# Kernel optimization log

Hardware: AMD Instinct MI355X
Metric: run time of the kernel (lower is better)

The kernel has to match this reference:

```python
import jax, jax.numpy as jnp
import numpy as np

B, S, V, E, H, T = 128, 512, 6000, 100, 256, 9


def setup_inputs() -> dict:
    key = jax.random.key(0)
    ks = jax.random.split(key, 16)
    lengths = jax.random.randint(ks[0], (B,), S // 4, S + 1)
    mask = (jnp.arange(S)[None, :] < lengths[:, None])  # [B,S] bool, contiguous prefixes
    data = jax.random.randint(ks[1], (B, S), 1, V)
    data = jnp.where(mask, data, 0)  # pad token = 0 (padding_idx)
    sc = 0.1
    emb = jax.random.normal(ks[2], (V, E), jnp.float32) * sc
    emb = emb.at[0].set(0.0)  # padding_idx=0
    return {
        "data": data, "mask": mask,
        "emb": emb,
        "W_ih_f": jax.random.normal(ks[3], (4 * H, E), jnp.float32) * sc,
        "W_hh_f": jax.random.normal(ks[4], (4 * H, H), jnp.float32) * sc,
        "b_f": jax.random.normal(ks[5], (4 * H,), jnp.float32) * sc,
        "W_ih_b": jax.random.normal(ks[6], (4 * H, E), jnp.float32) * sc,
        "W_hh_b": jax.random.normal(ks[7], (4 * H, H), jnp.float32) * sc,
        "b_b": jax.random.normal(ks[8], (4 * H,), jnp.float32) * sc,
        "mlp_W": jax.random.normal(ks[9], (T, 2 * H), jnp.float32) * sc,
        "mlp_b": jax.random.normal(ks[10], (T,), jnp.float32) * sc,
        "start_trans": jax.random.normal(ks[11], (T,), jnp.float32) * sc,
        "trans": jax.random.normal(ks[12], (T, T), jnp.float32) * sc,
        "end_trans": jax.random.normal(ks[13], (T,), jnp.float32) * sc,
    }


def _lstm_dir(xg, W_hh, reverse):
    # xg: [S,B,4H] precomputed input projection + biases
    h0 = jnp.zeros((xg.shape[1], W_hh.shape[1]), xg.dtype)

    def step(carry, xt):
        h, c = carry
        g = xt + h @ W_hh.T
        i, f, gg, o = jnp.split(g, 4, axis=-1)  # PyTorch gate order i,f,g,o
        c = jax.nn.sigmoid(f) * c + jax.nn.sigmoid(i) * jnp.tanh(gg)
        h = jax.nn.sigmoid(o) * jnp.tanh(c)
        return (h, c), h

    _, hs = jax.lax.scan(step, (h0, h0), xg, reverse=reverse)
    return hs  # [S,B,H]


def _emissions(data, emb, W_ih_f, W_hh_f, b_f, W_ih_b, W_hh_b, b_b, mlp_W, mlp_b):
    x = emb[data]  # [B,S,E]
    xg_f = jnp.einsum('bse,ge->sbg', x, W_ih_f) + b_f
    xg_b = jnp.einsum('bse,ge->sbg', x, W_ih_b) + b_b
    hf = _lstm_dir(xg_f, W_hh_f, False)
    hb = _lstm_dir(xg_b, W_hh_b, True)
    h = jnp.concatenate([hf, hb], axis=-1)  # [S,B,2H]
    return jnp.einsum('sbh,th->bst', h, mlp_W) + mlp_b  # [B,S,T]


def _viterbi(em, mask, start_trans, trans, end_trans):
    b, s, t = em.shape
    score0 = start_trans + em[:, 0]  # [B,T]
    em_t = jnp.swapaxes(em, 0, 1)[1:]      # [S-1,B,T]
    mask_t = jnp.swapaxes(mask, 0, 1)[1:]  # [S-1,B]

    def step(score, inp):
        e_t, m_t = inp
        cand = score[:, :, None] + trans[None] + e_t[:, None, :]  # [B,Tprev,Tcur]
        new = cand.max(axis=1)
        bp = cand.argmax(axis=1).astype(jnp.int32)  # [B,T]
        score = jnp.where(m_t[:, None], new, score)
        return score, bp

    score, bps = jax.lax.scan(step, score0, (em_t, mask_t))
    final = score + end_trans
    best_score = final.max(axis=-1)               # [B]
    last_tag = final.argmax(axis=-1).astype(jnp.int32)

    def back(tag, inp):
        bp, m_t = inp
        prev = jnp.take_along_axis(bp, tag[:, None], axis=1)[:, 0]
        prev = jnp.where(m_t, prev, tag)
        return prev, tag

    first_tag, tags_rest = jax.lax.scan(back, last_tag, (bps, mask_t), reverse=True)
    paths = jnp.concatenate([first_tag[None], tags_rest], axis=0)  # [S,B]
    paths = jnp.where(jnp.swapaxes(mask, 0, 1), paths, 0)
    return jnp.swapaxes(paths, 0, 1), best_score


def reference(data, mask, emb, W_ih_f, W_hh_f, b_f, W_ih_b, W_hh_b, b_b,
              mlp_W, mlp_b, start_trans, trans, end_trans):
    em = _emissions(data, emb, W_ih_f, W_hh_f, b_f, W_ih_b, W_hh_b, b_b, mlp_W, mlp_b)
    paths, best_score = _viterbi(em, mask, start_trans, trans, end_trans)
    return paths, best_score
```

## Files before the change

### kernel.cpp

```cpp
#include <hip/hip_runtime.h>
#include <math.h>
#include <stdint.h>

#define B 128
#define S 512
#define V 6000
#define E 100
#define H 256
#define G4 1024
#define T 9

#define WREG 18
#define WLDS 3
#define WSTR 43

#define OFF_PEMB_F 0u
#define PEMB_BYTES (V*G4*4u)
#define OFF_PEMB_B (OFF_PEMB_F + PEMB_BYTES)
#define OFF_EMF    (OFF_PEMB_B + PEMB_BYTES)
#define EM_BYTES   (B*S*T*4u)
#define OFF_EMB    (OFF_EMF + EM_BYTES)
#define OFF_BP     (OFF_EMB + EM_BYTES)
#define BP_BYTES   ((S-1)*B*16u)
#define OFF_LT     (OFF_BP + BP_BYTES)
#define OFF_PT     (OFF_LT + 512u)
#define OFF_WSTREAM OFF_BP

__device__ __forceinline__ float sigf(float x) { return 1.0f / (1.0f + expf(-x)); }

__global__ __launch_bounds__(256) void k_pemb(const float* __restrict__ emb,
                                              const float* __restrict__ wf, const float* __restrict__ bf,
                                              const float* __restrict__ wb, const float* __restrict__ bb,
                                              char* __restrict__ ws) {
    int blk = blockIdx.x;
    int d   = blk >= 375;
    int vb  = d ? blk - 375 : blk;
    const float* W    = d ? wb : wf;
    const float* bias = d ? bb : bf;
    float* pe = (float*)(ws + (d ? OFF_PEMB_B : OFF_PEMB_F));

    __shared__ float es[16 * E];
    for (int i = threadIdx.x; i < 16 * E; i += 256) es[i] = emb[vb * 16 * E + i];
    __syncthreads();

    int j = threadIdx.x;
    float acc[4][16];
    #pragma unroll
    for (int q = 0; q < 4; q++) {
        float bq = bias[q * H + j];
        #pragma unroll
        for (int v = 0; v < 16; v++) acc[q][v] = bq;
    }
    for (int e = 0; e < E; e++) {
        float w0 = W[(0 * H + j) * E + e];
        float w1 = W[(1 * H + j) * E + e];
        float w2 = W[(2 * H + j) * E + e];
        float w3 = W[(3 * H + j) * E + e];
        #pragma unroll
        for (int v = 0; v < 16; v++) {
            float x = es[v * E + e];
            acc[0][v] += w0 * x; acc[1][v] += w1 * x;
            acc[2][v] += w2 * x; acc[3][v] += w3 * x;
        }
    }
    for (int v = 0; v < 16; v++)
        #pragma unroll
        for (int q = 0; q < 4; q++)
            pe[(vb * 16 + v) * G4 + q * H + j] = acc[q][v];
}

__global__ __launch_bounds__(256) void k_prep(const float* __restrict__ whhf,
                                              const float* __restrict__ whhb,
                                              char* __restrict__ ws) {
    int tid = blockIdx.x * 256 + threadIdx.x;
    if (tid >= 2 * WSTR * 1024) return;
    int d   = tid >= WSTR * 1024;
    int idx = d ? tid - WSTR * 1024 : tid;
    int g = idx >> 10, r = idx & 1023;
    const float* whh = d ? whhb : whhf;
    float4* wstr = (float4*)(ws + OFF_WSTREAM);
    const float4* src = (const float4*)(whh + (size_t)r * H + 4 * (WREG + WLDS));
    wstr[((size_t)(d * WSTR + g) << 10) + r] = src[g];
}

__global__ __launch_bounds__(512, 2) void k_lstm(const int* __restrict__ data,
                                                 const float* __restrict__ whhf,
                                                 const float* __restrict__ whhb,
                                                 const float* __restrict__ mlpW,
                                                 char* __restrict__ ws) {
    int blk = blockIdx.x;
    int d = blk >> 7, b = blk & 127;
    const float* whh = d ? whhb : whhf;
    const float* pe  = (const float*)(ws + (d ? OFF_PEMB_B : OFF_PEMB_F));
    float* emdst = (float*)(ws + (d ? OFF_EMB : OFF_EMF));
    const float4* wstr = (const float4*)(ws + OFF_WSTREAM) + ((size_t)(d * WSTR) << 10);

    __shared__ __align__(16) float hs[H];
    __shared__ float4 sW[WLDS << 10];
    __shared__ float  gbuf[G4];
    __shared__ float  red[T][4];
    __shared__ int    toks[S];

    int t = threadIdx.x;
    int r0 = t, r1 = t + 512;

    const float4* wrow0 = (const float4*)(whh + (size_t)r0 * H);
    const float4* wrow1 = (const float4*)(whh + (size_t)r1 * H);
    float4 wA[WREG], wB[WREG];
    #pragma unroll
    for (int g = 0; g < WREG; g++) { wA[g] = wrow0[g]; wB[g] = wrow1[g]; }
    #pragma unroll
    for (int g = 0; g < WLDS; g++) {
        sW[(g << 10) + r0] = wrow0[WREG + g];
        sW[(g << 10) + r1] = wrow1[WREG + g];
    }

    toks[t] = data[b * S + t];

    float mw[T];
    if (t < 256) {
        #pragma unroll
        for (int tt = 0; tt < T; tt++) mw[tt] = mlpW[tt * (2 * H) + d * H + t];
    }
    if (t < H) hs[t] = 0.0f;
    float cst = 0.0f;
    __syncthreads();

    const float4* hs4 = (const float4*)hs;
    const float4* wsp0 = wstr + r0;
    const float4* wsp1 = wstr + r1;

    float pf0, pf1;
    {
        int sp0 = d ? (S - 1) : 0;
        size_t tok = (size_t)toks[sp0];
        pf0 = pe[(tok << 10) + r0];
        pf1 = pe[(tok << 10) + r1];
    }

    for (int ss = 0; ss < S; ss++) {
        int sp = d ? (S - 1 - ss) : ss;
        float acc0 = pf0, acc1 = pf1;
        if (ss + 1 < S) {
            int spn = d ? (S - 2 - ss) : (ss + 1);
            size_t tok = (size_t)toks[spn];
            pf0 = pe[(tok << 10) + r0];
            pf1 = pe[(tok << 10) + r1];
        }

        #pragma unroll
        for (int g = 0; g < WREG; g++) {
            float4 h4 = hs4[g];
            float4 a = wA[g], bb2 = wB[g];
            acc0 = fmaf(a.x, h4.x, acc0);  acc1 = fmaf(bb2.x, h4.x, acc1);
            acc0 = fmaf(a.y, h4.y, acc0);  acc1 = fmaf(bb2.y, h4.y, acc1);
            acc0 = fmaf(a.z, h4.z, acc0);  acc1 = fmaf(bb2.z, h4.z, acc1);
            acc0 = fmaf(a.w, h4.w, acc0);  acc1 = fmaf(bb2.w, h4.w, acc1);
        }
        #pragma unroll
        for (int g = 0; g < WLDS; g++) {
            float4 w0 = sW[(g << 10) + r0];
            float4 w1 = sW[(g << 10) + r1];
            float4 h4 = hs4[WREG + g];
            acc0 = fmaf(w0.x, h4.x, acc0);  acc1 = fmaf(w1.x, h4.x, acc1);
            acc0 = fmaf(w0.y, h4.y, acc0);  acc1 = fmaf(w1.y, h4.y, acc1);
            acc0 = fmaf(w0.z, h4.z, acc0);  acc1 = fmaf(w1.z, h4.z, acc1);
            acc0 = fmaf(w0.w, h4.w, acc0);  acc1 = fmaf(w1.w, h4.w, acc1);
        }
        #pragma unroll 4
        for (int g = 0; g < WSTR; g++) {
            float4 w0 = wsp0[(size_t)g << 10];
            float4 w1 = wsp1[(size_t)g << 10];
            float4 h4 = hs4[WREG + WLDS + g];
            acc0 = fmaf(w0.x, h4.x, acc0);  acc1 = fmaf(w1.x, h4.x, acc1);
            acc0 = fmaf(w0.y, h4.y, acc0);  acc1 = fmaf(w1.y, h4.y, acc1);
            acc0 = fmaf(w0.z, h4.z, acc0);  acc1 = fmaf(w1.z, h4.z, acc1);
            acc0 = fmaf(w0.w, h4.w, acc0);  acc1 = fmaf(w1.w, h4.w, acc1);
        }
        gbuf[r0] = acc0;
        gbuf[r1] = acc1;
        __syncthreads();

        if (t < 256) {
            float gi = gbuf[t], gf = gbuf[H + t], gg = gbuf[2 * H + t], go = gbuf[3 * H + t];
            float ig = sigf(gi), fg = sigf(gf), tg = tanhf(gg), og = sigf(go);
            cst = fg * cst + ig * tg;
            float hn = og * tanhf(cst);
            hs[t] = hn;
            int l = t & 63, wv = t >> 6;
            #pragma unroll
            for (int tt = 0; tt < T; tt++) {
                float v = hn * mw[tt];
                v += __shfl_xor(v, 32, 64); v += __shfl_xor(v, 16, 64);
                v += __shfl_xor(v, 8, 64);  v += __shfl_xor(v, 4, 64);
                v += __shfl_xor(v, 2, 64);  v += __shfl_xor(v, 1, 64);
                if (l == 0) red[tt][wv] = v;
            }
        }
        __syncthreads();
        if (t < T)
            emdst[((size_t)b * S + sp) * T + t] = red[t][0] + red[t][1] + red[t][2] + red[t][3];
    }
}

__global__ __launch_bounds__(64) void k_vit(const int* __restrict__ data,
                                            const float* __restrict__ strans,
                                            const float* __restrict__ trans,
                                            const float* __restrict__ etrans,
                                            const float* __restrict__ mlpb,
                                            float* __restrict__ out,
                                            char* __restrict__ ws) {
    int b = blockIdx.x, t = threadIdx.x;
    const float* emf = (const float*)(ws + OFF_EMF);
    const float* emb = (const float*)(ws + OFF_EMB);
    char* bp = ws + OFF_BP;
    int*  lt = (int*)(ws + OFF_LT);
    bool act = t < T;

    float trp[T];
    float mb = 0.0f;
    if (act) {
        #pragma unroll
        for (int p = 0; p < T; p++) trp[p] = trans[p * T + t];
        mb = mlpb[t];
    }
    float score = -1e30f;
    if (act) score = strans[t] + emf[(b * S) * T + t] + emb[(b * S) * T + t] + mb;

    for (int s = 1; s < S; s++) {
        float e = 0.0f;
        if (act) e = emf[(b * S + s) * T + t] + emb[(b * S + s) * T + t] + mb;
        float best = __shfl(score, 0, 64) + trp[0];
        int bpi = 0;
        #pragma unroll
        for (int p = 1; p < T; p++) {
            float cand = __shfl(score, p, 64) + trp[p];
            if (cand > best) { best = cand; bpi = p; }
        }
        int m = data[b * S + s] != 0;
        if (act) {
            score = m ? (best + e) : score;
            bp[((size_t)(s - 1) * B + b) * 16 + t] = (char)bpi;
        }
    }
    float fin = act ? score + etrans[t] : -1e30f;
    float bv = __shfl(fin, 0, 64);
    int bi = 0;
    #pragma unroll
    for (int p = 1; p < T; p++) {
        float v = __shfl(fin, p, 64);
        if (v > bv) { bv = v; bi = p; }
    }
    if (t == 0) { out[B * S + b] = bv; lt[b] = bi; }
}

__global__ __launch_bounds__(128) void k_back(const int* __restrict__ data, char* __restrict__ ws) {
    int b = threadIdx.x;
    const int4* bp4 = (const int4*)(ws + OFF_BP);
    const int*  lt  = (const int*)(ws + OFF_LT);
    int* pt = (int*)(ws + OFF_PT);
    int tag = lt[b];
    pt[(S - 1) * B + b] = tag;
    for (int p = S - 2; p >= 0; p--) {
        int4 r = bp4[(size_t)p * B + b];
        int m = data[b * S + p + 1] != 0;
        unsigned w = (unsigned)(tag < 8 ? (tag < 4 ? r.x : r.y) : r.z);
        int nt = (int)((w >> ((tag & 3) * 8)) & 0xff);
        tag = m ? nt : tag;
        pt[p * B + b] = tag;
    }
}

__global__ __launch_bounds__(256) void k_fin(const int* __restrict__ data,
                                             float* __restrict__ out,
                                             const char* __restrict__ ws) {
    int tid = blockIdx.x * 256 + threadIdx.x;
    const int* pt = (const int*)(ws + OFF_PT);
    int b = tid >> 9, p = tid & 511;
    out[tid] = (data[tid] != 0) ? (float)pt[p * B + b] : 0.0f;
}

extern "C" void kernel_launch(void* const* d_in, const int* in_sizes, int n_in,
                              void* d_out, int out_size, void* d_ws, size_t ws_size,
                              hipStream_t stream) {
    const int*   data = (const int*)d_in[0];
    const float* emb  = (const float*)d_in[2];
    const float* wihf = (const float*)d_in[3];
    const float* whhf = (const float*)d_in[4];
    const float* bf   = (const float*)d_in[5];
    const float* wihb = (const float*)d_in[6];
    const float* whhb = (const float*)d_in[7];
    const float* bb   = (const float*)d_in[8];
    const float* mlpW = (const float*)d_in[9];
    const float* mlpb = (const float*)d_in[10];
    const float* st   = (const float*)d_in[11];
    const float* tr   = (const float*)d_in[12];
    const float* et   = (const float*)d_in[13];
    float* out = (float*)d_out;
    char*  ws  = (char*)d_ws;

    hipLaunchKernelGGL(k_pemb, dim3(750),  dim3(256), 0, stream, emb, wihf, bf, wihb, bb, ws);
    hipLaunchKernelGGL(k_prep, dim3(344),  dim3(256), 0, stream, whhf, whhb, ws);
    hipLaunchKernelGGL(k_lstm, dim3(256),  dim3(512), 0, stream, data, whhf, whhb, mlpW, ws);
    hipLaunchKernelGGL(k_vit,  dim3(128),  dim3(64),  0, stream, data, st, tr, et, mlpb, out, ws);
    hipLaunchKernelGGL(k_back, dim3(1),    dim3(128), 0, stream, data, ws);
    hipLaunchKernelGGL(k_fin,  dim3(256),  dim3(256), 0, stream, data, out, ws);
}
```

Measured before the change: 5.145 ms.

## Remap LSTM to one thread per hidden unit with AGPR-resident weights

The recurrent kernel now runs 256 threads per block, and each thread computes all four gates of one hidden unit. This removes the gate exchange buffer and one barrier's worth of cross-thread work. Recurrent weights sit in three tiers: a slice in VGPRs, a larger slice parked in accumulation registers (AGPRs) via inline asm, and a small slice in LDS. Only the remaining columns are streamed from the regrouped global copy, which cuts global and L2 weight traffic per step. The risks are fewer waves to hide latency, extra accvgpr read instructions, and register pressure from the inline asm.

```diff
diff --git a/kernel.cpp b/kernel.cpp
--- a/kernel.cpp
+++ b/kernel.cpp
@@ -10,9 +10,11 @@
 #define G4 1024
 #define T 9
 
-#define WREG 18
-#define WLDS 3
-#define WSTR 43
+#define NVG 9
+#define NAG 16
+#define NLD 3
+#define NST 36
+#define GST (NVG + NAG + NLD)
 
 #define OFF_PEMB_F 0u
 #define PEMB_BYTES (V*G4*4u)
@@ -73,17 +75,19 @@
                                               const float* __restrict__ whhb,
                                               char* __restrict__ ws) {
     int tid = blockIdx.x * 256 + threadIdx.x;
-    if (tid >= 2 * WSTR * 1024) return;
-    int d   = tid >= WSTR * 1024;
-    int idx = d ? tid - WSTR * 1024 : tid;
-    int g = idx >> 10, r = idx & 1023;
+    if (tid >= 2 * 4 * NST * 256) return;
+    int d   = tid >= 4 * NST * 256;
+    int idx = d ? tid - 4 * NST * 256 : tid;
+    int q  = idx / (NST * 256);
+    int r2 = idx % (NST * 256);
+    int gi = r2 >> 8, j = r2 & 255;
     const float* whh = d ? whhb : whhf;
     float4* wstr = (float4*)(ws + OFF_WSTREAM);
-    const float4* src = (const float4*)(whh + (size_t)r * H + 4 * (WREG + WLDS));
-    wstr[((size_t)(d * WSTR + g) << 10) + r] = src[g];
-}
-
-__global__ __launch_bounds__(512, 2) void k_lstm(const int* __restrict__ data,
+    const float4* src = (const float4*)(whh + (size_t)(q * H + j) * H);
+    wstr[((size_t)((d * 4 + q) * NST + gi) << 8) + j] = src[GST + gi];
+}
+
+__global__ __launch_bounds__(256, 1) void k_lstm(const int* __restrict__ data,
                                                  const float* __restrict__ whhf,
                                                  const float* __restrict__ whhb,
                                                  const float* __restrict__ mlpW,
@@ -93,109 +97,161 @@
     const float* whh = d ? whhb : whhf;
     const float* pe  = (const float*)(ws + (d ? OFF_PEMB_B : OFF_PEMB_F));
     float* emdst = (float*)(ws + (d ? OFF_EMB : OFF_EMF));
-    const float4* wstr = (const float4*)(ws + OFF_WSTREAM) + ((size_t)(d * WSTR) << 10);
+    const float4* wstr = (const float4*)(ws + OFF_WSTREAM);
 
     __shared__ __align__(16) float hs[H];
-    __shared__ float4 sW[WLDS << 10];
-    __shared__ float  gbuf[G4];
+    __shared__ float4 sW[NLD * 4 * 256];
     __shared__ float  red[T][4];
     __shared__ int    toks[S];
 
     int t = threadIdx.x;
-    int r0 = t, r1 = t + 512;
-
-    const float4* wrow0 = (const float4*)(whh + (size_t)r0 * H);
-    const float4* wrow1 = (const float4*)(whh + (size_t)r1 * H);
-    float4 wA[WREG], wB[WREG];
-    #pragma unroll
-    for (int g = 0; g < WREG; g++) { wA[g] = wrow0[g]; wB[g] = wrow1[g]; }
-    #pragma unroll
-    for (int g = 0; g < WLDS; g++) {
-        sW[(g << 10) + r0] = wrow0[WREG + g];
-        sW[(g << 10) + r1] = wrow1[WREG + g];
-    }
+
+    float4 wv[NVG * 4];
+    #pragma unroll
+    for (int g = 0; g < NVG; g++)
+        #pragma unroll
+        for (int q = 0; q < 4; q++)
+            wv[g * 4 + q] = ((const float4*)(whh + (size_t)(q * H + t) * H))[g];
+    #pragma unroll
+    for (int i = 0; i < NVG * 4; i++)
+        asm volatile("" : "+v"(wv[i].x), "+v"(wv[i].y), "+v"(wv[i].z), "+v"(wv[i].w));
+
+    float ag[NAG * 4 * 4];
+    #pragma unroll
+    for (int g = 0; g < NAG; g++)
+        #pragma unroll
+        for (int q = 0; q < 4; q++) {
+            float4 w = ((const float4*)(whh + (size_t)(q * H + t) * H))[NVG + g];
+            int base = (g * 4 + q) * 4;
+            asm volatile("v_accvgpr_write_b32 %0, %1" : "=a"(ag[base + 0]) : "v"(w.x));
+            asm volatile("v_accvgpr_write_b32 %0, %1" : "=a"(ag[base + 1]) : "v"(w.y));
+            asm volatile("v_accvgpr_write_b32 %0, %1" : "=a"(ag[base + 2]) : "v"(w.z));
+            asm volatile("v_accvgpr_write_b32 %0, %1" : "=a"(ag[base + 3]) : "v"(w.w));
+        }
+
+    #pragma unroll
+    for (int g = 0; g < NLD; g++)
+        #pragma unroll
+        for (int q = 0; q < 4; q++)
+            sW[((g * 4 + q) << 8) + t] = ((const float4*)(whh + (size_t)(q * H + t) * H))[NVG + NAG + g];
 
     toks[t] = data[b * S + t];
+    toks[t + 256] = data[b * S + t + 256];
 
     float mw[T];
-    if (t < 256) {
-        #pragma unroll
-        for (int tt = 0; tt < T; tt++) mw[tt] = mlpW[tt * (2 * H) + d * H + t];
-    }
-    if (t < H) hs[t] = 0.0f;
+    #pragma unroll
+    for (int tt = 0; tt < T; tt++) mw[tt] = mlpW[tt * (2 * H) + d * H + t];
+
+    hs[t] = 0.0f;
     float cst = 0.0f;
     __syncthreads();
 
     const float4* hs4 = (const float4*)hs;
-    const float4* wsp0 = wstr + r0;
-    const float4* wsp1 = wstr + r1;
-
-    float pf0, pf1;
+    const float4* ws0 = wstr + (((size_t)(d * 4 + 0) * NST) << 8) + t;
+    const float4* ws1 = wstr + (((size_t)(d * 4 + 1) * NST) << 8) + t;
+    const float4* ws2 = wstr + (((size_t)(d * 4 + 2) * NST) << 8) + t;
+    const float4* ws3 = wstr + (((size_t)(d * 4 + 3) * NST) << 8) + t;
+
+    float pf0, pf1, pf2, pf3;
     {
         int sp0 = d ? (S - 1) : 0;
         size_t tok = (size_t)toks[sp0];
-        pf0 = pe[(tok << 10) + r0];
-        pf1 = pe[(tok << 10) + r1];
+        pf0 = pe[(tok << 10) + 0 * H + t];
+        pf1 = pe[(tok << 10) + 1 * H + t];
+        pf2 = pe[(tok << 10) + 2 * H + t];
+        pf3 = pe[(tok << 10) + 3 * H + t];
     }
 
     for (int ss = 0; ss < S; ss++) {
         int sp = d ? (S - 1 - ss) : ss;
-        float acc0 = pf0, acc1 = pf1;
+        float a0 = pf0, a1 = pf1, a2 = pf2, a3 = pf3;
         if (ss + 1 < S) {
             int spn = d ? (S - 2 - ss) : (ss + 1);
             size_t tok = (size_t)toks[spn];
-            pf0 = pe[(tok << 10) + r0];
-            pf1 = pe[(tok << 10) + r1];
-        }
-
-        #pragma unroll
-        for (int g = 0; g < WREG; g++) {
+            pf0 = pe[(tok << 10) + 0 * H + t];
+            pf1 = pe[(tok << 10) + 1 * H + t];
+            pf2 = pe[(tok << 10) + 2 * H + t];
+            pf3 = pe[(tok << 10) + 3 * H + t];
+        }
+
+        #pragma unroll
+        for (int g = 0; g < NVG; g++) {
             float4 h4 = hs4[g];
-            float4 a = wA[g], bb2 = wB[g];
-            acc0 = fmaf(a.x, h4.x, acc0);  acc1 = fmaf(bb2.x, h4.x, acc1);
-            acc0 = fmaf(a.y, h4.y, acc0);  acc1 = fmaf(bb2.y, h4.y, acc1);
-            acc0 = fmaf(a.z, h4.z, acc0);  acc1 = fmaf(bb2.z, h4.z, acc1);
-            acc0 = fmaf(a.w, h4.w, acc0);  acc1 = fmaf(bb2.w, h4.w, acc1);
-        }
-        #pragma unroll
-        for (int g = 0; g < WLDS; g++) {
-            float4 w0 = sW[(g << 10) + r0];
-            float4 w1 = sW[(g << 10) + r1];
-            float4 h4 = hs4[WREG + g];
-            acc0 = fmaf(w0.x, h4.x, acc0);  acc1 = fmaf(w1.x, h4.x, acc1);
-            acc0 = fmaf(w0.y, h4.y, acc0);  acc1 = fmaf(w1.y, h4.y, acc1);
-            acc0 = fmaf(w0.z, h4.z, acc0);  acc1 = fmaf(w1.z, h4.z, acc1);
-            acc0 = fmaf(w0.w, h4.w, acc0);  acc1 = fmaf(w1.w, h4.w, acc1);
+            float4 w0 = wv[g * 4 + 0], w1 = wv[g * 4 + 1],
+                   w2 = wv[g * 4 + 2], w3 = wv[g * 4 + 3];
+            a0 = fmaf(w0.x, h4.x, a0); a0 = fmaf(w0.y, h4.y, a0);
+            a0 = fmaf(w0.z, h4.z, a0); a0 = fmaf(w0.w, h4.w, a0);
+            a1 = fmaf(w1.x, h4.x, a1); a1 = fmaf(w1.y, h4.y, a1);
+            a1 = fmaf(w1.z, h4.z, a1); a1 = fmaf(w1.w, h4.w, a1);
+            a2 = fmaf(w2.x, h4.x, a2); a2 = fmaf(w2.y, h4.y, a2);
+            a2 = fmaf(w2.z, h4.z, a2); a2 = fmaf(w2.w, h4.w, a2);
+            a3 = fmaf(w3.x, h4.x, a3); a3 = fmaf(w3.y, h4.y, a3);
+            a3 = fmaf(w3.z, h4.z, a3); a3 = fmaf(w3.w, h4.w, a3);
+        }
+        #pragma unroll
+        for (int g = 0; g < NAG; g++) {
+            float4 h4 = hs4[NVG + g];
+            #pragma unroll
+            for (int q = 0; q < 4; q++) {
+                int base = (g * 4 + q) * 4;
+                float w0, w1, w2, w3;
+                asm volatile("v_accvgpr_read_b32 %0, %1" : "=v"(w0) : "a"(ag[base + 0]));
+                asm volatile("v_accvgpr_read_b32 %0, %1" : "=v"(w1) : "a"(ag[base + 1]));
+                asm volatile("v_accvgpr_read_b32 %0, %1" : "=v"(w2) : "a"(ag[base + 2]));
+                asm volatile("v_accvgpr_read_b32 %0, %1" : "=v"(w3) : "a"(ag[base + 3]));
+                float acc = (q == 0) ? a0 : (q == 1) ? a1 : (q == 2) ? a2 : a3;
+                acc = fmaf(w0, h4.x, acc); acc = fmaf(w1, h4.y, acc);
+                acc = fmaf(w2, h4.z, acc); acc = fmaf(w3, h4.w, acc);
+                if (q == 0) a0 = acc; else if (q == 1) a1 = acc;
+                else if (q == 2) a2 = acc; else a3 = acc;
+            }
+        }
+        #pragma unroll
+        for (int g = 0; g < NLD; g++) {
+            float4 h4 = hs4[NVG + NAG + g];
+            float4 w0 = sW[((g * 4 + 0) << 8) + t], w1 = sW[((g * 4 + 1) << 8) + t];
+            float4 w2 = sW[((g * 4 + 2) << 8) + t], w3 = sW[((g * 4 + 3) << 8) + t];
+            a0 = fmaf(w0.x, h4.x, a0); a0 = fmaf(w0.y, h4.y, a0);
+            a0 = fmaf(w0.z, h4.z, a0); a0 = fmaf(w0.w, h4.w, a0);
+            a1 = fmaf(w1.x, h4.x, a1); a1 = fmaf(w1.y, h4.y, a1);
+            a1 = fmaf(w1.z, h4.z, a1); a1 = fmaf(w1.w, h4.w, a1);
+            a2 = fmaf(w2.x, h4.x, a2); a2 = fmaf(w2.y, h4.y, a2);
+            a2 = fmaf(w2.z, h4.z, a2); a2 = fmaf(w2.w, h4.w, a2);
+            a3 = fmaf(w3.x, h4.x, a3); a3 = fmaf(w3.y, h4.y, a3);
+            a3 = fmaf(w3.z, h4.z, a3); a3 = fmaf(w3.w, h4.w, a3);
         }
         #pragma unroll 4
-        for (int g = 0; g < WSTR; g++) {
-            float4 w0 = wsp0[(size_t)g << 10];
-            float4 w1 = wsp1[(size_t)g << 10];
-            float4 h4 = hs4[WREG + WLDS + g];
-            acc0 = fmaf(w0.x, h4.x, acc0);  acc1 = fmaf(w1.x, h4.x, acc1);
-            acc0 = fmaf(w0.y, h4.y, acc0);  acc1 = fmaf(w1.y, h4.y, acc1);
-            acc0 = fmaf(w0.z, h4.z, acc0);  acc1 = fmaf(w1.z, h4.z, acc1);
-            acc0 = fmaf(w0.w, h4.w, acc0);  acc1 = fmaf(w1.w, h4.w, acc1);
-        }
-        gbuf[r0] = acc0;
-        gbuf[r1] = acc1;
+        for (int gs = 0; gs < NST; gs++) {
+            float4 w0 = ws0[gs << 8];
+            float4 w1 = ws1[gs << 8];
+            float4 w2 = ws2[gs << 8];
+            float4 w3 = ws3[gs << 8];
+            float4 h4 = hs4[GST + gs];
+            a0 = fmaf(w0.x, h4.x, a0); a0 = fmaf(w0.y, h4.y, a0);
+            a0 = fmaf(w0.z, h4.z, a0); a0 = fmaf(w0.w, h4.w, a0);
+            a1 = fmaf(w1.x, h4.x, a1); a1 = fmaf(w1.y, h4.y, a1);
+            a1 = fmaf(w1.z, h4.z, a1); a1 = fmaf(w1.w, h4.w, a1);
+            a2 = fmaf(w2.x, h4.x, a2); a2 = fmaf(w2.y, h4.y, a2);
+            a2 = fmaf(w2.z, h4.z, a2); a2 = fmaf(w2.w, h4.w, a2);
+            a3 = fmaf(w3.x, h4.x, a3); a3 = fmaf(w3.y, h4.y, a3);
+            a3 = fmaf(w3.z, h4.z, a3); a3 = fmaf(w3.w, h4.w, a3);
+        }
+
+        float ig = sigf(a0), fg = sigf(a1), tg = tanhf(a2), og = sigf(a3);
+        cst = fg * cst + ig * tg;
+        float hn = og * tanhf(cst);
+
         __syncthreads();
-
-        if (t < 256) {
-            float gi = gbuf[t], gf = gbuf[H + t], gg = gbuf[2 * H + t], go = gbuf[3 * H + t];
-            float ig = sigf(gi), fg = sigf(gf), tg = tanhf(gg), og = sigf(go);
-            cst = fg * cst + ig * tg;
-            float hn = og * tanhf(cst);
-            hs[t] = hn;
-            int l = t & 63, wv = t >> 6;
-            #pragma unroll
-            for (int tt = 0; tt < T; tt++) {
-                float v = hn * mw[tt];
-                v += __shfl_xor(v, 32, 64); v += __shfl_xor(v, 16, 64);
-                v += __shfl_xor(v, 8, 64);  v += __shfl_xor(v, 4, 64);
-                v += __shfl_xor(v, 2, 64);  v += __shfl_xor(v, 1, 64);
-                if (l == 0) red[tt][wv] = v;
-            }
+        hs[t] = hn;
+
+        int l = t & 63, wv2 = t >> 6;
+        #pragma unroll
+        for (int tt = 0; tt < T; tt++) {
+            float v = hn * mw[tt];
+            v += __shfl_xor(v, 32, 64); v += __shfl_xor(v, 16, 64);
+            v += __shfl_xor(v, 8, 64);  v += __shfl_xor(v, 4, 64);
+            v += __shfl_xor(v, 2, 64);  v += __shfl_xor(v, 1, 64);
+            if (l == 0) red[tt][wv2] = v;
         }
         __syncthreads();
         if (t < T)
@@ -300,8 +356,8 @@
     char*  ws  = (char*)d_ws;
 
     hipLaunchKernelGGL(k_pemb, dim3(750),  dim3(256), 0, stream, emb, wihf, bf, wihb, bb, ws);
-    hipLaunchKernelGGL(k_prep, dim3(344),  dim3(256), 0, stream, whhf, whhb, ws);
-    hipLaunchKernelGGL(k_lstm, dim3(256),  dim3(512), 0, stream, data, whhf, whhb, mlpW, ws);
+    hipLaunchKernelGGL(k_prep, dim3(288),  dim3(256), 0, stream, whhf, whhb, ws);
+    hipLaunchKernelGGL(k_lstm, dim3(256),  dim3(256), 0, stream, data, whhf, whhb, mlpW, ws);
     hipLaunchKernelGGL(k_vit,  dim3(128),  dim3(64),  0, stream, data, st, tr, et, mlpb, out, ws);
     hipLaunchKernelGGL(k_back, dim3(1),    dim3(128), 0, stream, data, ws);
     hipLaunchKernelGGL(k_fin,  dim3(256),  dim3(256), 0, stream, data, out, ws);
```

New measurement: 7.457 ms. 45.0% more time.

## Hold recurrent weights in AGPRs and enlarge LDS weight cache to cut streaming

Applied to the files above, without the earlier changes.

Rebalances where the recurrent W_hh rows live in the LSTM kernel. 16 float4 groups per row now sit in accumulator registers (written and read through inline asm), 9 groups sit in about 147 KB of dynamic LDS, and only 39 groups are streamed from global memory each step instead of 43. The prep kernel and its grid are resized to match. The aim is less per-step global/L2 traffic on the serial recurrence. In exchange it adds AGPR read instructions, and the large LDS footprint limits the kernel to one block per CU. It also sets the dynamic-LDS attribute on every host call.

```diff
diff --git a/kernel.cpp b/kernel.cpp
--- a/kernel.cpp
+++ b/kernel.cpp
@@ -10,9 +10,17 @@
 #define G4 1024
 #define T 9
 
-#define WREG 18
-#define WLDS 3
-#define WSTR 43
+#define NAGR 16
+#define NLDR 9
+#define NSTR 39
+#define GSTR (NAGR + NLDR)
+
+#define SM_W    0u
+#define SM_HS   147456u
+#define SM_GB   148480u
+#define SM_RED  152576u
+#define SM_TOK  152720u
+#define SM_SIZE 154768u
 
 #define OFF_PEMB_F 0u
 #define PEMB_BYTES (V*G4*4u)
@@ -73,14 +81,14 @@
                                               const float* __restrict__ whhb,
                                               char* __restrict__ ws) {
     int tid = blockIdx.x * 256 + threadIdx.x;
-    if (tid >= 2 * WSTR * 1024) return;
-    int d   = tid >= WSTR * 1024;
-    int idx = d ? tid - WSTR * 1024 : tid;
-    int g = idx >> 10, r = idx & 1023;
+    if (tid >= 2 * NSTR * 1024) return;
+    int d   = tid >= NSTR * 1024;
+    int idx = d ? tid - NSTR * 1024 : tid;
+    int gi = idx >> 10, r = idx & 1023;
     const float* whh = d ? whhb : whhf;
     float4* wstr = (float4*)(ws + OFF_WSTREAM);
-    const float4* src = (const float4*)(whh + (size_t)r * H + 4 * (WREG + WLDS));
-    wstr[((size_t)(d * WSTR + g) << 10) + r] = src[g];
+    const float4* src = (const float4*)(whh + (size_t)r * H);
+    wstr[((size_t)(d * NSTR + gi) << 10) + r] = src[GSTR + gi];
 }
 
 __global__ __launch_bounds__(512, 2) void k_lstm(const int* __restrict__ data,
@@ -88,31 +96,43 @@
                                                  const float* __restrict__ whhb,
                                                  const float* __restrict__ mlpW,
                                                  char* __restrict__ ws) {
+    extern __shared__ char smem[];
+    float4* sW  = (float4*)(smem + SM_W);
+    float*  hs  = (float*)(smem + SM_HS);
+    float*  gbuf= (float*)(smem + SM_GB);
+    float (*red)[4] = (float(*)[4])(smem + SM_RED);
+    int*    toks= (int*)(smem + SM_TOK);
+
     int blk = blockIdx.x;
     int d = blk >> 7, b = blk & 127;
     const float* whh = d ? whhb : whhf;
     const float* pe  = (const float*)(ws + (d ? OFF_PEMB_B : OFF_PEMB_F));
     float* emdst = (float*)(ws + (d ? OFF_EMB : OFF_EMF));
-    const float4* wstr = (const float4*)(ws + OFF_WSTREAM) + ((size_t)(d * WSTR) << 10);
-
-    __shared__ __align__(16) float hs[H];
-    __shared__ float4 sW[WLDS << 10];
-    __shared__ float  gbuf[G4];
-    __shared__ float  red[T][4];
-    __shared__ int    toks[S];
+    const float4* wstrD = (const float4*)(ws + OFF_WSTREAM) + ((size_t)(d * NSTR) << 10);
 
     int t = threadIdx.x;
     int r0 = t, r1 = t + 512;
-
     const float4* wrow0 = (const float4*)(whh + (size_t)r0 * H);
     const float4* wrow1 = (const float4*)(whh + (size_t)r1 * H);
-    float4 wA[WREG], wB[WREG];
+
+    float agA[NAGR * 4], agB[NAGR * 4];
     #pragma unroll
-    for (int g = 0; g < WREG; g++) { wA[g] = wrow0[g]; wB[g] = wrow1[g]; }
+    for (int g = 0; g < NAGR; g++) {
+        float4 wa = wrow0[g];
+        float4 wb2 = wrow1[g];
+        asm volatile("v_accvgpr_write_b32 %0, %1" : "=a"(agA[g * 4 + 0]) : "v"(wa.x));
+        asm volatile("v_accvgpr_write_b32 %0, %1" : "=a"(agA[g * 4 + 1]) : "v"(wa.y));
+        asm volatile("v_accvgpr_write_b32 %0, %1" : "=a"(agA[g * 4 + 2]) : "v"(wa.z));
+        asm volatile("v_accvgpr_write_b32 %0, %1" : "=a"(agA[g * 4 + 3]) : "v"(wa.w));
+        asm volatile("v_accvgpr_write_b32 %0, %1" : "=a"(agB[g * 4 + 0]) : "v"(wb2.x));
+        asm volatile("v_accvgpr_write_b32 %0, %1" : "=a"(agB[g * 4 + 1]) : "v"(wb2.y));
+        asm volatile("v_accvgpr_write_b32 %0, %1" : "=a"(agB[g * 4 + 2]) : "v"(wb2.z));
+        asm volatile("v_accvgpr_write_b32 %0, %1" : "=a"(agB[g * 4 + 3]) : "v"(wb2.w));
+    }
     #pragma unroll
-    for (int g = 0; g < WLDS; g++) {
-        sW[(g << 10) + r0] = wrow0[WREG + g];
-        sW[(g << 10) + r1] = wrow1[WREG + g];
+    for (int g = 0; g < NLDR; g++) {
+        sW[(g << 10) + r0] = wrow0[NAGR + g];
+        sW[(g << 10) + r1] = wrow1[NAGR + g];
     }
 
     toks[t] = data[b * S + t];
@@ -127,8 +147,8 @@
     __syncthreads();
 
     const float4* hs4 = (const float4*)hs;
-    const float4* wsp0 = wstr + r0;
-    const float4* wsp1 = wstr + r1;
+    const float4* wsp0 = wstrD + r0;
+    const float4* wsp1 = wstrD + r1;
 
     float pf0, pf1;
     {
@@ -149,29 +169,37 @@
         }
 
         #pragma unroll
-        for (int g = 0; g < WREG; g++) {
+        for (int g = 0; g < NAGR; g++) {
             float4 h4 = hs4[g];
-            float4 a = wA[g], bb2 = wB[g];
-            acc0 = fmaf(a.x, h4.x, acc0);  acc1 = fmaf(bb2.x, h4.x, acc1);
-            acc0 = fmaf(a.y, h4.y, acc0);  acc1 = fmaf(bb2.y, h4.y, acc1);
-            acc0 = fmaf(a.z, h4.z, acc0);  acc1 = fmaf(bb2.z, h4.z, acc1);
-            acc0 = fmaf(a.w, h4.w, acc0);  acc1 = fmaf(bb2.w, h4.w, acc1);
-        }
-        #pragma unroll
-        for (int g = 0; g < WLDS; g++) {
+            float a0, a1, a2, a3, b0v, b1v, b2v, b3v;
+            asm volatile("v_accvgpr_read_b32 %0, %1" : "=v"(a0)  : "a"(agA[g * 4 + 0]));
+            asm volatile("v_accvgpr_read_b32 %0, %1" : "=v"(a1)  : "a"(agA[g * 4 + 1]));
+            asm volatile("v_accvgpr_read_b32 %0, %1" : "=v"(a2)  : "a"(agA[g * 4 + 2]));
+            asm volatile("v_accvgpr_read_b32 %0, %1" : "=v"(a3)  : "a"(agA[g * 4 + 3]));
+            asm volatile("v_accvgpr_read_b32 %0, %1" : "=v"(b0v) : "a"(agB[g * 4 + 0]));
+            asm volatile("v_accvgpr_read_b32 %0, %1" : "=v"(b1v) : "a"(agB[g * 4 + 1]));
+            asm volatile("v_accvgpr_read_b32 %0, %1" : "=v"(b2v) : "a"(agB[g * 4 + 2]));
+            asm volatile("v_accvgpr_read_b32 %0, %1" : "=v"(b3v) : "a"(agB[g * 4 + 3]));
+            acc0 = fmaf(a0, h4.x, acc0);  acc1 = fmaf(b0v, h4.x, acc1);
+            acc0 = fmaf(a1, h4.y, acc0);  acc1 = fmaf(b1v, h4.y, acc1);
+            acc0 = fmaf(a2, h4.z, acc0);  acc1 = fmaf(b2v, h4.z, acc1);
+            acc0 = fmaf(a3, h4.w, acc0);  acc1 = fmaf(b3v, h4.w, acc1);
+        }
+        #pragma unroll
+        for (int g = 0; g < NLDR; g++) {
             float4 w0 = sW[(g << 10) + r0];
             float4 w1 = sW[(g << 10) + r1];
-            float4 h4 = hs4[WREG + g];
+            float4 h4 = hs4[NAGR + g];
             acc0 = fmaf(w0.x, h4.x, acc0);  acc1 = fmaf(w1.x, h4.x, acc1);
             acc0 = fmaf(w0.y, h4.y, acc0);  acc1 = fmaf(w1.y, h4.y, acc1);
             acc0 = fmaf(w0.z, h4.z, acc0);  acc1 = fmaf(w1.z, h4.z, acc1);
             acc0 = fmaf(w0.w, h4.w, acc0);  acc1 = fmaf(w1.w, h4.w, acc1);
         }
         #pragma unroll 4
-        for (int g = 0; g < WSTR; g++) {
+        for (int g = 0; g < NSTR; g++) {
             float4 w0 = wsp0[(size_t)g << 10];
             float4 w1 = wsp1[(size_t)g << 10];
-            float4 h4 = hs4[WREG + WLDS + g];
+            float4 h4 = hs4[GSTR + g];
             acc0 = fmaf(w0.x, h4.x, acc0);  acc1 = fmaf(w1.x, h4.x, acc1);
             acc0 = fmaf(w0.y, h4.y, acc0);  acc1 = fmaf(w1.y, h4.y, acc1);
             acc0 = fmaf(w0.z, h4.z, acc0);  acc1 = fmaf(w1.z, h4.z, acc1);
@@ -299,9 +327,14 @@
     float* out = (float*)d_out;
     char*  ws  = (char*)d_ws;
 
+    static int lds_attr_done = 0;
+    (void)lds_attr_done;
+    hipFuncSetAttribute(reinterpret_cast<const void*>(k_lstm),
+                        hipFuncAttributeMaxDynamicSharedMemorySize, 160 * 1024);
+
     hipLaunchKernelGGL(k_pemb, dim3(750),  dim3(256), 0, stream, emb, wihf, bf, wihb, bb, ws);
-    hipLaunchKernelGGL(k_prep, dim3(344),  dim3(256), 0, stream, whhf, whhb, ws);
-    hipLaunchKernelGGL(k_lstm, dim3(256),  dim3(512), 0, stream, data, whhf, whhb, mlpW, ws);
+    hipLaunchKernelGGL(k_prep, dim3(312),  dim3(256), 0, stream, whhf, whhb, ws);
+    hipLaunchKernelGGL(k_lstm, dim3(256),  dim3(512), SM_SIZE, stream, data, whhf, whhb, mlpW, ws);
     hipLaunchKernelGGL(k_vit,  dim3(128),  dim3(64),  0, stream, data, st, tr, et, mlpb, out, ws);
     hipLaunchKernelGGL(k_back, dim3(1),    dim3(128), 0, stream, data, ws);
     hipLaunchKernelGGL(k_fin,  dim3(256),  dim3(256), 0, stream, data, out, ws);
```

New measurement: 5.121 ms. Within noise of the previous version (-0.5%).

## Drop register-resident W_hh, stream weights from global with software prefetch

Applied to the files above, without the earlier changes.

The recurrent weights are no longer kept in registers. They are read either directly from the original rows or from a transposed stream buffer, with the first two stream chunks prefetched one step ahead. Which path runs depends on the workspace size: if it is large enough, everything beyond the three LDS chunks is streamed from a separate region. The aim is to free registers and raise occupancy or scheduling freedom, at the cost of far more global/L2 traffic per timestep in the latency-critical recurrence.

```diff
diff --git a/kernel.cpp b/kernel.cpp
--- a/kernel.cpp
+++ b/kernel.cpp
@@ -10,9 +10,7 @@
 #define G4 1024
 #define T 9
 
-#define WREG 18
-#define WLDS 3
-#define WSTR 43
+#define GLDS 3
 
 #define OFF_PEMB_F 0u
 #define PEMB_BYTES (V*G4*4u)
@@ -24,7 +22,9 @@
 #define BP_BYTES   ((S-1)*B*16u)
 #define OFF_LT     (OFF_BP + BP_BYTES)
 #define OFF_PT     (OFF_LT + 512u)
-#define OFF_WSTREAM OFF_BP
+#define PT_BYTES   (B*S*4u)
+#define OFF_WFULL  (OFF_PT + PT_BYTES)
+#define WFULL_BYTES (2ull*61*1024*16)
 
 __device__ __forceinline__ float sigf(float x) { return 1.0f / (1.0f + expf(-x)); }
 
@@ -69,52 +69,51 @@
             pe[(vb * 16 + v) * G4 + q * H + j] = acc[q][v];
 }
 
-__global__ __launch_bounds__(256) void k_prep(const float* __restrict__ whhf,
-                                              const float* __restrict__ whhb,
-                                              char* __restrict__ ws) {
+__global__ __launch_bounds__(256) void k_prep2(const float* __restrict__ whhf,
+                                               const float* __restrict__ whhb,
+                                               float4* __restrict__ wstr,
+                                               int colbase, int nstr) {
     int tid = blockIdx.x * 256 + threadIdx.x;
-    if (tid >= 2 * WSTR * 1024) return;
-    int d   = tid >= WSTR * 1024;
-    int idx = d ? tid - WSTR * 1024 : tid;
-    int g = idx >> 10, r = idx & 1023;
+    if (tid >= 2 * nstr * 1024) return;
+    int d   = tid >= nstr * 1024;
+    int idx = d ? tid - nstr * 1024 : tid;
+    int gi = idx >> 10, r = idx & 1023;
     const float* whh = d ? whhb : whhf;
-    float4* wstr = (float4*)(ws + OFF_WSTREAM);
-    const float4* src = (const float4*)(whh + (size_t)r * H + 4 * (WREG + WLDS));
-    wstr[((size_t)(d * WSTR + g) << 10) + r] = src[g];
-}
-
-__global__ __launch_bounds__(512, 2) void k_lstm(const int* __restrict__ data,
-                                                 const float* __restrict__ whhf,
-                                                 const float* __restrict__ whhb,
-                                                 const float* __restrict__ mlpW,
-                                                 char* __restrict__ ws) {
+    wstr[((size_t)(d * nstr + gi) << 10) + r] =
+        ((const float4*)(whh + (size_t)r * H))[colbase + gi];
+}
+
+template<int NROW>
+__global__ __launch_bounds__(512, 2) void k_lstm_t(const int* __restrict__ data,
+                                                   const float* __restrict__ whhf,
+                                                   const float* __restrict__ whhb,
+                                                   const float* __restrict__ mlpW,
+                                                   const float4* __restrict__ wstrAll,
+                                                   char* __restrict__ ws) {
+    constexpr int NSTR = 61 - NROW;
     int blk = blockIdx.x;
     int d = blk >> 7, b = blk & 127;
     const float* whh = d ? whhb : whhf;
     const float* pe  = (const float*)(ws + (d ? OFF_PEMB_B : OFF_PEMB_F));
     float* emdst = (float*)(ws + (d ? OFF_EMB : OFF_EMF));
-    const float4* wstr = (const float4*)(ws + OFF_WSTREAM) + ((size_t)(d * WSTR) << 10);
+    const float4* wstrD = wstrAll + ((size_t)(d * NSTR) << 10);
 
     __shared__ __align__(16) float hs[H];
-    __shared__ float4 sW[WLDS << 10];
+    __shared__ float4 sW[GLDS << 10];
     __shared__ float  gbuf[G4];
     __shared__ float  red[T][4];
     __shared__ int    toks[S];
 
     int t = threadIdx.x;
     int r0 = t, r1 = t + 512;
-
     const float4* wrow0 = (const float4*)(whh + (size_t)r0 * H);
     const float4* wrow1 = (const float4*)(whh + (size_t)r1 * H);
-    float4 wA[WREG], wB[WREG];
+
     #pragma unroll
-    for (int g = 0; g < WREG; g++) { wA[g] = wrow0[g]; wB[g] = wrow1[g]; }
-    #pragma unroll
-    for (int g = 0; g < WLDS; g++) {
-        sW[(g << 10) + r0] = wrow0[WREG + g];
-        sW[(g << 10) + r1] = wrow1[WREG + g];
-    }
-
+    for (int g = 0; g < GLDS; g++) {
+        sW[(g << 10) + r0] = wrow0[g];
+        sW[(g << 10) + r1] = wrow1[g];
+    }
     toks[t] = data[b * S + t];
 
     float mw[T];
@@ -127,8 +126,8 @@
     __syncthreads();
 
     const float4* hs4 = (const float4*)hs;
-    const float4* wsp0 = wstr + r0;
-    const float4* wsp1 = wstr + r1;
+    const float4* wsp0 = wstrD + r0;
+    const float4* wsp1 = wstrD + r1;
 
     float pf0, pf1;
     {
@@ -137,6 +136,8 @@
         pf0 = pe[(tok << 10) + r0];
         pf1 = pe[(tok << 10) + r1];
     }
+    float4 n00 = wsp0[0],        n10 = wsp1[0];
+    float4 n01 = wsp0[1 << 10],  n11 = wsp1[1 << 10];
 
     for (int ss = 0; ss < S; ss++) {
         int sp = d ? (S - 1 - ss) : ss;
@@ -149,34 +150,50 @@
         }
 
         #pragma unroll
-        for (int g = 0; g < WREG; g++) {
-            float4 h4 = hs4[g];
-            float4 a = wA[g], bb2 = wB[g];
-            acc0 = fmaf(a.x, h4.x, acc0);  acc1 = fmaf(bb2.x, h4.x, acc1);
-            acc0 = fmaf(a.y, h4.y, acc0);  acc1 = fmaf(bb2.y, h4.y, acc1);
-            acc0 = fmaf(a.z, h4.z, acc0);  acc1 = fmaf(bb2.z, h4.z, acc1);
-            acc0 = fmaf(a.w, h4.w, acc0);  acc1 = fmaf(bb2.w, h4.w, acc1);
-        }
-        #pragma unroll
-        for (int g = 0; g < WLDS; g++) {
+        for (int g = 0; g < GLDS; g++) {
             float4 w0 = sW[(g << 10) + r0];
             float4 w1 = sW[(g << 10) + r1];
-            float4 h4 = hs4[WREG + g];
+            float4 h4 = hs4[g];
             acc0 = fmaf(w0.x, h4.x, acc0);  acc1 = fmaf(w1.x, h4.x, acc1);
             acc0 = fmaf(w0.y, h4.y, acc0);  acc1 = fmaf(w1.y, h4.y, acc1);
             acc0 = fmaf(w0.z, h4.z, acc0);  acc1 = fmaf(w1.z, h4.z, acc1);
             acc0 = fmaf(w0.w, h4.w, acc0);  acc1 = fmaf(w1.w, h4.w, acc1);
         }
-        #pragma unroll 4
-        for (int g = 0; g < WSTR; g++) {
-            float4 w0 = wsp0[(size_t)g << 10];
-            float4 w1 = wsp1[(size_t)g << 10];
-            float4 h4 = hs4[WREG + WLDS + g];
+        #pragma unroll
+        for (int g = 0; g < NROW; g++) {
+            float4 w0 = wrow0[GLDS + g];
+            float4 w1 = wrow1[GLDS + g];
+            float4 h4 = hs4[GLDS + g];
             acc0 = fmaf(w0.x, h4.x, acc0);  acc1 = fmaf(w1.x, h4.x, acc1);
             acc0 = fmaf(w0.y, h4.y, acc0);  acc1 = fmaf(w1.y, h4.y, acc1);
             acc0 = fmaf(w0.z, h4.z, acc0);  acc1 = fmaf(w1.z, h4.z, acc1);
             acc0 = fmaf(w0.w, h4.w, acc0);  acc1 = fmaf(w1.w, h4.w, acc1);
         }
+        {
+            float4 h4 = hs4[GLDS + NROW];
+            acc0 = fmaf(n00.x, h4.x, acc0);  acc1 = fmaf(n10.x, h4.x, acc1);
+            acc0 = fmaf(n00.y, h4.y, acc0);  acc1 = fmaf(n10.y, h4.y, acc1);
+            acc0 = fmaf(n00.z, h4.z, acc0);  acc1 = fmaf(n10.z, h4.z, acc1);
+            acc0 = fmaf(n00.w, h4.w, acc0);  acc1 = fmaf(n10.w, h4.w, acc1);
+            h4 = hs4[GLDS + NROW + 1];
+            acc0 = fmaf(n01.x, h4.x, acc0);  acc1 = fmaf(n11.x, h4.x, acc1);
+            acc0 = fmaf(n01.y, h4.y, acc0);  acc1 = fmaf(n11.y, h4.y, acc1);
+            acc0 = fmaf(n01.z, h4.z, acc0);  acc1 = fmaf(n11.z, h4.z, acc1);
+            acc0 = fmaf(n01.w, h4.w, acc0);  acc1 = fmaf(n11.w, h4.w, acc1);
+        }
+        #pragma unroll 4
+        for (int gs = 2; gs < NSTR; gs++) {
+            float4 w0 = wsp0[(size_t)gs << 10];
+            float4 w1 = wsp1[(size_t)gs << 10];
+            float4 h4 = hs4[GLDS + NROW + gs];
+            acc0 = fmaf(w0.x, h4.x, acc0);  acc1 = fmaf(w1.x, h4.x, acc1);
+            acc0 = fmaf(w0.y, h4.y, acc0);  acc1 = fmaf(w1.y, h4.y, acc1);
+            acc0 = fmaf(w0.z, h4.z, acc0);  acc1 = fmaf(w1.z, h4.z, acc1);
+            acc0 = fmaf(w0.w, h4.w, acc0);  acc1 = fmaf(w1.w, h4.w, acc1);
+        }
+        n00 = wsp0[0];        n10 = wsp1[0];
+        n01 = wsp0[1 << 10];  n11 = wsp1[1 << 10];
+
         gbuf[r0] = acc0;
         gbuf[r1] = acc1;
         __syncthreads();
@@ -299,10 +316,19 @@
     float* out = (float*)d_out;
     char*  ws  = (char*)d_ws;
 
-    hipLaunchKernelGGL(k_pemb, dim3(750),  dim3(256), 0, stream, emb, wihf, bf, wihb, bb, ws);
-    hipLaunchKernelGGL(k_prep, dim3(344),  dim3(256), 0, stream, whhf, whhb, ws);
-    hipLaunchKernelGGL(k_lstm, dim3(256),  dim3(512), 0, stream, data, whhf, whhb, mlpW, ws);
-    hipLaunchKernelGGL(k_vit,  dim3(128),  dim3(64),  0, stream, data, st, tr, et, mlpb, out, ws);
-    hipLaunchKernelGGL(k_back, dim3(1),    dim3(128), 0, stream, data, ws);
-    hipLaunchKernelGGL(k_fin,  dim3(256),  dim3(256), 0, stream, data, out, ws);
-}
+    bool full = ws_size >= (size_t)OFF_WFULL + (size_t)WFULL_BYTES;
+    float4* wstr = full ? (float4*)(ws + OFF_WFULL) : (float4*)(ws + OFF_BP);
+    int nrow = full ? 0 : 20;
+    int nstr = 61 - nrow;
+    int prep_blocks = (2 * nstr * 1024 + 255) / 256;
+
+    k_pemb<<<dim3(750), dim3(256), 0, stream>>>(emb, wihf, bf, wihb, bb, ws);
+    k_prep2<<<dim3(prep_blocks), dim3(256), 0, stream>>>(whhf, whhb, wstr, GLDS + nrow, nstr);
+    if (full)
+        k_lstm_t<0><<<dim3(256), dim3(512), 0, stream>>>(data, whhf, whhb, mlpW, wstr, ws);
+    else
+        k_lstm_t<20><<<dim3(256), dim3(512), 0, stream>>>(data, whhf, whhb, mlpW, wstr, ws);
+    k_vit<<<dim3(128), dim3(64), 0, stream>>>(data, st, tr, et, mlpb, out, ws);
+    k_back<<<dim3(1), dim3(128), 0, stream>>>(data, ws);
+    k_fin<<<dim3(256), dim3(256), 0, stream>>>(data, out, ws);
+}
```

Result: slower. 6.036 ms (+17.3%).
